# Kernel tuning notes

Measured on AMD Instinct MI355X. Metric: run time of the kernel, lower is better.

The kernel has to match this reference:

```python
import jax, jax.numpy as jnp
import numpy as np

BETA = 0.95
THR = 1.0
T = 50        # NUM_TIME_STEPS
L = 2         # SNN_NUM_LAYERS
SLOPE = 25.0  # fast_sigmoid surrogate slope

@jax.custom_vjp
def spike(v):
    # Heaviside on (mem - threshold) with fast_sigmoid surrogate gradient
    return (v > 0).astype(v.dtype)

def _spike_fwd(v):
    return (v > 0).astype(v.dtype), v

def _spike_bwd(v, g):
    return (g / (SLOPE * jnp.abs(v) + 1.0) ** 2,)

spike.defvjp(_spike_fwd, _spike_bwd)


def setup_inputs() -> dict:
    key = jax.random.key(0)
    k1, k2, _ = jax.random.split(key, 3)
    B, IN, H = 4096, 512, 1024
    x = jax.random.normal(k1, (B, IN), dtype=jnp.float32)
    W_proj = jax.random.normal(k2, (IN, H), dtype=jnp.float32) / np.sqrt(IN).astype(np.float32)
    b_proj = jnp.zeros((H,), dtype=jnp.float32)
    return {"x": x, "W_proj": W_proj, "b_proj": b_proj}


def reference(x, W_proj, b_proj):
    # Static input current fed at every time step (input_features != hidden -> Linear projection)
    inp = x @ W_proj + b_proj                         # [B, H]
    B, H = inp.shape

    def step(carry, _):
        mems, agg, tot = carry
        new_mems = []
        for li in range(L):  # independent LIF layers, all driven by the same static input
            mem = mems[li]
            # snnTorch Leaky (reset_mechanism='subtract'):
            reset = spike(mem - THR)                  # reset based on previous mem
            mem = BETA * mem + inp - reset * THR      # leaky integration + subtractive reset
            spk = spike(mem - THR)                    # output spike from new mem
            new_mems.append(mem)
            tot = tot + spk.sum(axis=1)               # total spikes per sample (all layers)
            if li == L - 1:
                agg = agg + spk                       # sum of last-layer spikes over time
        return (tuple(new_mems), agg, tot), None

    init = (
        tuple(jnp.zeros((B, H), inp.dtype) for _ in range(L)),  # init_leaky -> zeros
        jnp.zeros((B, H), inp.dtype),
        jnp.zeros((B,), inp.dtype),
    )
    (mems, agg, tot), _ = jax.lax.scan(step, init, None, length=T)
    return agg, tot
```

## Files before the change

### kernel.cpp

```cpp
#include <hip/hip_runtime.h>
#include <stdint.h>

#define MDIM 4096
#define NDIM 1024
#define KDIM 512
#define TSTEPS 50
#define NCH 16

typedef _Float16 half8 __attribute__((ext_vector_type(8)));
typedef float    f32x4 __attribute__((ext_vector_type(4)));

typedef const __attribute__((address_space(1))) void cgv_t;
typedef __attribute__((address_space(3))) void lv_t;

__device__ __forceinline__ void gload16(const void* g, void* s) {
    __builtin_amdgcn_global_load_lds((cgv_t*)g, (lv_t*)s, 16, 0, 0);
}

__global__ __launch_bounds__(256) void split_kernel(
    const float* __restrict__ A, const float* __restrict__ W,
    char* __restrict__ A1, char* __restrict__ A2,
    char* __restrict__ B1, char* __restrict__ B2,
    float* __restrict__ tot)
{
    const int blk = blockIdx.x;
    if (blk < 1024) {
        int idx = blk * 256 + threadIdx.x;
        if (idx < MDIM) tot[idx] = 0.0f;
        int r = idx >> 6, q = idx & 63, c = q >> 2, lg = q & 3;
        const float* pA = A + (size_t)r * KDIM + c * 32 + lg * 8;
        float4 v0 = *(const float4*)pA;
        float4 v1 = *(const float4*)(pA + 4);
        float v[8] = {v0.x, v0.y, v0.z, v0.w, v1.x, v1.y, v1.z, v1.w};
        half8 h1, h2;
        #pragma unroll
        for (int e = 0; e < 8; ++e) {
            h1[e] = (_Float16)v[e];
            h2[e] = (_Float16)((v[e] - (float)h1[e]) * 2048.0f);
        }
        int off = (r >> 6) * 65536 + c * 4096 + lg * 1024
                + (((r & 63) ^ (lg << 1)) << 4);
        *(half8*)(A1 + off) = h1;
        *(half8*)(A2 + off) = h2;
    } else {
        int idx = (blk - 1024) * 256 + threadIdx.x;
        int q = idx >> 10, n = idx & 1023, c = q >> 2, lg = q & 3;
        float v[8];
        #pragma unroll
        for (int e = 0; e < 8; ++e)
            v[e] = W[(size_t)(c * 32 + lg * 8 + e) * NDIM + n];
        half8 h1, h2;
        #pragma unroll
        for (int e = 0; e < 8; ++e) {
            h1[e] = (_Float16)v[e];
            h2[e] = (_Float16)((v[e] - (float)h1[e]) * 2048.0f);
        }
        int off = (n >> 6) * 65536 + c * 4096 + lg * 1024
                + (((n & 63) ^ (lg << 1)) << 4);
        *(half8*)(B1 + off) = h1;
        *(half8*)(B2 + off) = h2;
    }
}

__global__ __launch_bounds__(256, 4) void snn_mfma_kernel(
    const char* __restrict__ A1, const char* __restrict__ A2,
    const char* __restrict__ B1, const char* __restrict__ B2,
    const float* __restrict__ bias, float* __restrict__ agg, float* __restrict__ tot)
{
    __shared__ __align__(16) unsigned char lds[2][16384];

    const int t  = threadIdx.x;
    const int l  = t & 63;
    const int w  = t >> 6;
    const int li = l & 15;
    const int lg = l >> 4;
    const int qr = (w >> 1) * 32;
    const int qc = (w & 1) * 32;

    const int swz = (blockIdx.x & 7) * 128 + (blockIdx.x >> 3);
    const int m0 = (swz >> 4) * 64;
    const int n0 = (swz & 15) * 64;

    const int aoff = (m0 >> 6) * 65536 + w * 1024 + l * 16;
    const int boff = (n0 >> 6) * 65536 + w * 1024 + l * 16;
    const int dstw = w * 1024;

#define STAGE(buf, ch) do {                                                   \
    const int c_ = (ch) * 4096;                                               \
    gload16(A1 + aoff + c_, &lds[buf][dstw]);                                 \
    gload16(A2 + aoff + c_, &lds[buf][4096  + dstw]);                         \
    gload16(B1 + boff + c_, &lds[buf][8192  + dstw]);                         \
    gload16(B2 + boff + c_, &lds[buf][12288 + dstw]);                         \
} while (0)

    int aL[2], bL[2];
    #pragma unroll
    for (int i = 0; i < 2; ++i) {
        aL[i] = lg * 1024 + (((qr + i * 16 + li) ^ (lg << 1)) << 4);
        bL[i] = lg * 1024 + (((qc + i * 16 + li) ^ (lg << 1)) << 4);
    }

    f32x4 acc_lo[2][2], acc_hi[2][2];
    #pragma unroll
    for (int i = 0; i < 2; ++i)
        #pragma unroll
        for (int j = 0; j < 2; ++j) {
            acc_lo[i][j] = (f32x4){0.f, 0.f, 0.f, 0.f};
            acc_hi[i][j] = (f32x4){0.f, 0.f, 0.f, 0.f};
        }

    STAGE(0, 0);
    STAGE(1, 1);

    #pragma unroll 1
    for (int ch = 0; ch < NCH; ++ch) {
        if (ch < NCH - 1) asm volatile("s_waitcnt vmcnt(4)" ::: "memory");
        else              asm volatile("s_waitcnt vmcnt(0)" ::: "memory");
        __builtin_amdgcn_s_barrier();
        asm volatile("" ::: "memory");
        const unsigned char* sb = lds[ch & 1];

        half8 af1[2], af2[2], bf1[2], bf2[2];
        #pragma unroll
        for (int i = 0; i < 2; ++i) {
            af1[i] = *(const half8*)(sb + aL[i]);
            af2[i] = *(const half8*)(sb + 4096 + aL[i]);
            bf1[i] = *(const half8*)(sb + 8192 + bL[i]);
            bf2[i] = *(const half8*)(sb + 12288 + bL[i]);
        }
        #pragma unroll
        for (int i = 0; i < 2; ++i)
            #pragma unroll
            for (int j = 0; j < 2; ++j)
                acc_hi[i][j] = __builtin_amdgcn_mfma_f32_16x16x32_f16(
                    af2[i], bf1[j], acc_hi[i][j], 0, 0, 0);
        #pragma unroll
        for (int i = 0; i < 2; ++i)
            #pragma unroll
            for (int j = 0; j < 2; ++j)
                acc_hi[i][j] = __builtin_amdgcn_mfma_f32_16x16x32_f16(
                    af1[i], bf2[j], acc_hi[i][j], 0, 0, 0);
        #pragma unroll
        for (int i = 0; i < 2; ++i)
            #pragma unroll
            for (int j = 0; j < 2; ++j)
                acc_lo[i][j] = __builtin_amdgcn_mfma_f32_16x16x32_f16(
                    af1[i], bf1[j], acc_lo[i][j], 0, 0, 0);

        __builtin_amdgcn_s_barrier();
        asm volatile("" ::: "memory");
        if (ch + 2 < NCH) STAGE(ch & 1, ch + 2);
    }

    float cb[2];
    #pragma unroll
    for (int j = 0; j < 2; ++j) cb[j] = bias[n0 + qc + j * 16 + li];

    #pragma unroll
    for (int i = 0; i < 2; ++i) {
        int rsum[4] = {0, 0, 0, 0};
        #pragma unroll
        for (int j = 0; j < 2; ++j) {
            float c[4], c1[4], mem[4];
            int cnt[4];
            bool sp[4];
            #pragma unroll
            for (int r = 0; r < 4; ++r) {
                c[r]   = fmaf(acc_hi[i][j][r], 4.8828125e-4f, acc_lo[i][j][r])
                       + cb[j];
                c1[r]  = c[r] - 1.0f;
                mem[r] = 0.0f;
                cnt[r] = 0;
                sp[r]  = false;
            }
            #pragma unroll 1
            for (int tt = 0; tt < TSTEPS; ++tt) {
                #pragma unroll
                for (int r = 0; r < 4; ++r) {
                    mem[r] = fmaf(0.95f, mem[r], sp[r] ? c1[r] : c[r]);
                    sp[r]  = mem[r] > 1.0f;
                    cnt[r] += sp[r] ? 1 : 0;
                }
            }
            const int col = n0 + qc + j * 16 + li;
            #pragma unroll
            for (int r = 0; r < 4; ++r) {
                const int row = m0 + qr + i * 16 + lg * 4 + r;
                agg[(size_t)row * NDIM + col] = (float)cnt[r];
                rsum[r] += cnt[r];
            }
        }
        #pragma unroll
        for (int r = 0; r < 4; ++r) {
            int s = rsum[r];
            s += __shfl_xor(s, 1);
            s += __shfl_xor(s, 2);
            s += __shfl_xor(s, 4);
            s += __shfl_xor(s, 8);
            if (li == 0)
                atomicAdd(&tot[m0 + qr + i * 16 + lg * 4 + r], 2.0f * (float)s);
        }
        __builtin_amdgcn_sched_barrier(0);
    }
}

extern "C" void kernel_launch(void* const* d_in, const int* in_sizes, int n_in,
                              void* d_out, int out_size, void* d_ws, size_t ws_size,
                              hipStream_t stream) {
    const float* x = (const float*)d_in[0];
    const float* W = (const float*)d_in[1];
    const float* b = (const float*)d_in[2];
    float* agg = (float*)d_out;
    float* tot = agg + (size_t)MDIM * NDIM;

    char* ws = (char*)d_ws;
    char* A1 = ws;
    char* A2 = ws + (4 << 20);
    char* B1 = ws + (8 << 20);
    char* B2 = ws + (9 << 20);

    split_kernel<<<1024 + 256, 256, 0, stream>>>(x, W, A1, A2, B1, B2,
                                                 (float*)tot);
    snn_mfma_kernel<<<(MDIM / 64) * (NDIM / 64), 256, 0, stream>>>(
        A1, A2, B1, B2, b, agg, tot);
}
```

Before: 54.44 us.

## Enlarge GEMM block tile to 128x64 with 512 threads sharing B

Each workgroup now covers a 128-row by 64-column output tile using 8 waves, so the B-operand chunks staged into LDS are shared by twice as many rows. Staging is redistributed so each wave issues three 16-byte global-to-LDS loads per chunk, and the wait count is adjusted to match. The aim is less global and L2 traffic for B and fewer blocks in total. The cost is a larger LDS footprint and bigger workgroups, which may lower occupancy and make barriers more expensive.

```diff
diff --git a/kernel.cpp b/kernel.cpp
--- a/kernel.cpp
+++ b/kernel.cpp
@@ -38,7 +38,7 @@
             h1[e] = (_Float16)v[e];
             h2[e] = (_Float16)((v[e] - (float)h1[e]) * 2048.0f);
         }
-        int off = (r >> 6) * 65536 + c * 4096 + lg * 1024
+        int off = ((r >> 6) * 16 + c) * 4096 + lg * 1024
                 + (((r & 63) ^ (lg << 1)) << 4);
         *(half8*)(A1 + off) = h1;
         *(half8*)(A2 + off) = h2;
@@ -55,19 +55,19 @@
             h1[e] = (_Float16)v[e];
             h2[e] = (_Float16)((v[e] - (float)h1[e]) * 2048.0f);
         }
-        int off = (n >> 6) * 65536 + c * 4096 + lg * 1024
+        int off = ((n >> 6) * 16 + c) * 4096 + lg * 1024
                 + (((n & 63) ^ (lg << 1)) << 4);
         *(half8*)(B1 + off) = h1;
         *(half8*)(B2 + off) = h2;
     }
 }
 
-__global__ __launch_bounds__(256, 4) void snn_mfma_kernel(
+__global__ __launch_bounds__(512, 4) void snn_mfma_kernel(
     const char* __restrict__ A1, const char* __restrict__ A2,
     const char* __restrict__ B1, const char* __restrict__ B2,
     const float* __restrict__ bias, float* __restrict__ agg, float* __restrict__ tot)
 {
-    __shared__ __align__(16) unsigned char lds[2][16384];
+    __shared__ __align__(16) unsigned char lds[2][24576];
 
     const int t  = threadIdx.x;
     const int l  = t & 63;
@@ -77,27 +77,46 @@
     const int qr = (w >> 1) * 32;
     const int qc = (w & 1) * 32;
 
-    const int swz = (blockIdx.x & 7) * 128 + (blockIdx.x >> 3);
-    const int m0 = (swz >> 4) * 64;
+    const int swz = (blockIdx.x & 7) * 64 + (blockIdx.x >> 3);
+    const int m0 = (swz >> 4) * 128;
     const int n0 = (swz & 15) * 64;
 
-    const int aoff = (m0 >> 6) * 65536 + w * 1024 + l * 16;
-    const int boff = (n0 >> 6) * 65536 + w * 1024 + l * 16;
-    const int dstw = w * 1024;
+    const char* ssrc[3];
+    int sdst[3];
+    #pragma unroll
+    for (int s_ = 0; s_ < 3; ++s_) {
+        const int s = w * 3 + s_;
+        const char* img;
+        int band, lg_, dst;
+        if (s < 16) {
+            img  = (s < 8) ? A1 : A2;
+            band = (s & 7) >> 2;
+            lg_  = s & 3;
+            dst  = ((s < 8) ? 0 : 8192) + band * 4096 + lg_ * 1024;
+            ssrc[s_] = img + (size_t)(((m0 >> 6) + band) * 16) * 4096
+                           + lg_ * 1024 + l * 16;
+        } else {
+            img  = (s < 20) ? B1 : B2;
+            lg_  = s & 3;
+            dst  = ((s < 20) ? 16384 : 20480) + lg_ * 1024;
+            ssrc[s_] = img + (size_t)((n0 >> 6) * 16) * 4096
+                           + lg_ * 1024 + l * 16;
+        }
+        sdst[s_] = dst;
+    }
 
 #define STAGE(buf, ch) do {                                                   \
-    const int c_ = (ch) * 4096;                                               \
-    gload16(A1 + aoff + c_, &lds[buf][dstw]);                                 \
-    gload16(A2 + aoff + c_, &lds[buf][4096  + dstw]);                         \
-    gload16(B1 + boff + c_, &lds[buf][8192  + dstw]);                         \
-    gload16(B2 + boff + c_, &lds[buf][12288 + dstw]);                         \
+    _Pragma("unroll") for (int s_ = 0; s_ < 3; ++s_)                          \
+        gload16(ssrc[s_] + (size_t)(ch) * 4096, &lds[buf][sdst[s_]]);         \
 } while (0)
 
-    int aL[2], bL[2];
+    int aF[2], bF[2];
     #pragma unroll
     for (int i = 0; i < 2; ++i) {
-        aL[i] = lg * 1024 + (((qr + i * 16 + li) ^ (lg << 1)) << 4);
-        bL[i] = lg * 1024 + (((qc + i * 16 + li) ^ (lg << 1)) << 4);
+        const int rbase = qr + i * 16;
+        aF[i] = ((rbase >> 6) * 4096) + lg * 1024
+              + ((((rbase & 63) + li) ^ (lg << 1)) << 4);
+        bF[i] = lg * 1024 + (((qc + i * 16 + li) ^ (lg << 1)) << 4);
     }
 
     f32x4 acc_lo[2][2], acc_hi[2][2];
@@ -114,7 +133,7 @@
 
     #pragma unroll 1
     for (int ch = 0; ch < NCH; ++ch) {
-        if (ch < NCH - 1) asm volatile("s_waitcnt vmcnt(4)" ::: "memory");
+        if (ch < NCH - 1) asm volatile("s_waitcnt vmcnt(3)" ::: "memory");
         else              asm volatile("s_waitcnt vmcnt(0)" ::: "memory");
         __builtin_amdgcn_s_barrier();
         asm volatile("" ::: "memory");
@@ -123,10 +142,10 @@
         half8 af1[2], af2[2], bf1[2], bf2[2];
         #pragma unroll
         for (int i = 0; i < 2; ++i) {
-            af1[i] = *(const half8*)(sb + aL[i]);
-            af2[i] = *(const half8*)(sb + 4096 + aL[i]);
-            bf1[i] = *(const half8*)(sb + 8192 + bL[i]);
-            bf2[i] = *(const half8*)(sb + 12288 + bL[i]);
+            af1[i] = *(const half8*)(sb + aF[i]);
+            af2[i] = *(const half8*)(sb + 8192 + aF[i]);
+            bf1[i] = *(const half8*)(sb + 16384 + bF[i]);
+            bf2[i] = *(const half8*)(sb + 20480 + bF[i]);
         }
         #pragma unroll
         for (int i = 0; i < 2; ++i)
@@ -221,6 +240,6 @@
 
     split_kernel<<<1024 + 256, 256, 0, stream>>>(x, W, A1, A2, B1, B2,
                                                  (float*)tot);
-    snn_mfma_kernel<<<(MDIM / 64) * (NDIM / 64), 256, 0, stream>>>(
+    snn_mfma_kernel<<<(MDIM / 128) * (NDIM / 64), 512, 0, stream>>>(
         A1, A2, B1, B2, b, agg, tot);
 }
```

Measured after the change: 53.74 us. No clear change (-1.3%).
